# Optimization experiments

Measured on AMD Instinct MI355X. Metric: run time of the kernel, lower is better.

The kernel has to match this reference:

```python
import jax, jax.numpy as jnp
import numpy as np

KNN_K = 10        # init kwarg knn_k
EPS_COS = 1e-8    # torch F.cosine_similarity default eps
EPS_SCALE = 1e-6  # clamp on median displacement variance


def _knn_indices(pts, k):
    """pts: [B, P, 3]. Returns [B, P, k] indices of nearest points.

    Matches torch: topk over negative squared pairwise distance (self point
    has distance 0 and is therefore included among the neighbors).
    """
    inner = jnp.einsum('bpd,bqd->bpq', pts, pts)            # [B,P,P]
    xx = jnp.sum(pts * pts, axis=-1)                        # [B,P]
    neg_dist = 2.0 * inner - xx[:, :, None] - xx[:, None, :]
    return jax.lax.top_k(neg_dist, k)[1]                    # [B,P,k]


def setup_inputs() -> dict:
    key = jax.random.key(0)
    k1, k2 = jax.random.split(key)
    B, D, T, P = 4, 128, 8, 4096
    return {
        'encoded': jax.random.normal(k1, (B, D, T * P), dtype=jnp.float32),
        'points_4d': jax.random.normal(k2, (B, T, P, 4), dtype=jnp.float32),
        'num_frames': T,
        'pts_per_frame': P,
    }


def reference(encoded, points_4d, num_frames, pts_per_frame):
    B, D, _ = encoded.shape
    xyz = points_4d[..., :3]                                # [B,T,P,3]
    feat = encoded.reshape(B, D, num_frames, pts_per_frame)
    k = min(KNN_K, pts_per_frame - 1)
    gather = jax.vmap(lambda a, i: a[i])                    # per-batch fancy gather

    total = jnp.asarray(0.0, dtype=encoded.dtype)
    for t in range(num_frames - 1):                         # small fixed frame loop
        pts = xyz[:, t]                                     # [B,P,3]
        disp = xyz[:, t + 1] - pts                          # [B,P,3]
        idx = _knn_indices(pts, k)                          # [B,P,k]

        nbr_disp = gather(disp, idx)                        # [B,P,k,3]
        disp_diff = nbr_disp - disp[:, :, None, :]
        disp_var = jnp.mean(jnp.sum(disp_diff * disp_diff, axis=-1), axis=-1)  # [B,P]

        # torch .median() on even-length returns the lower middle element
        flat = jnp.sort(disp_var.reshape(-1))
        scale = jnp.maximum(flat[(flat.shape[0] - 1) // 2], EPS_SCALE)
        rigidity = jax.lax.stop_gradient(jnp.exp(-disp_var / scale))  # detached

        feat_t = jnp.transpose(feat[:, :, t], (0, 2, 1))    # [B,P,D]
        nbr_feat = gather(feat_t, idx)                      # [B,P,k,D]
        num = jnp.einsum('bpd,bpkd->bpk', feat_t, nbr_feat)
        nq = jnp.maximum(jnp.linalg.norm(feat_t, axis=-1), EPS_COS)   # [B,P]
        nn_ = jnp.maximum(jnp.linalg.norm(nbr_feat, axis=-1), EPS_COS)  # [B,P,k]
        cos_sim = num / (nq[:, :, None] * nn_)
        mean_sim = jnp.mean(cos_sim, axis=-1)               # [B,P]

        total = total + jnp.mean(rigidity * (1.0 - mean_sim))
    return total / max(num_frames - 1, 1)
```

## Files before the change

### kernel.cpp

```cpp
#include <hip/hip_runtime.h>
#include <math.h>

#define BB 4
#define DD 128
#define TT 8
#define PP 4096
#define KK 10
#define NT 7
#define BP (BB*PP)
#define NQ (NT*BP)
#define NBLK_COS 896
#define QPB 128

#define CHUNKS 4
#define CSZ (PP/CHUNKS)
#define SELCAP 16

#define OFF_FEATT 0u
#define OFF_PARTV 0u
#define OFF_CAND4 20971520u
#define OFF_IDX   58720256u
#define OFF_DV    63307776u
#define OFF_NORM  63766528u
#define OFF_SCALE 64225280u
#define OFF_PART  64225536u

typedef __fp16 f16x2 __attribute__((ext_vector_type(2)));
union H2U { f16x2 h; unsigned u; };

__device__ __forceinline__ float md_of(const float4 q, const float4 c) {
  float s = q.w + c.w;
  float inner = fmaf(q.x, c.x, fmaf(q.y, c.y, q.z * c.z));
  return fmaf(-2.0f, inner, s);
}

__device__ __forceinline__ void ins2(f16x2 (&bv)[KK], float mdA, float mdB) {
  H2U cv;
  cv.h = __builtin_amdgcn_cvt_pkrtz(mdA, mdB);
  cv.u += 0x00020002u;
  bv[KK - 1] = __builtin_elementwise_min(bv[KK - 1], cv.h);
#pragma unroll
  for (int i = KK - 1; i > 0; --i) {
    f16x2 lo = __builtin_elementwise_min(bv[i - 1], bv[i]);
    f16x2 hi = __builtin_elementwise_max(bv[i - 1], bv[i]);
    bv[i - 1] = lo;
    bv[i] = hi;
  }
}
__device__ __forceinline__ void insh(f16x2 (&bv)[KK], f16x2 h) {
  bv[KK - 1] = __builtin_elementwise_min(bv[KK - 1], h);
#pragma unroll
  for (int i = KK - 1; i > 0; --i) {
    f16x2 lo = __builtin_elementwise_min(bv[i - 1], bv[i]);
    f16x2 hi = __builtin_elementwise_max(bv[i - 1], bv[i]);
    bv[i - 1] = lo;
    bv[i] = hi;
  }
}

__device__ __forceinline__ void insf(float (&bv)[KK], float v) {
  bv[KK - 1] = fminf(bv[KK - 1], v);
#pragma unroll
  for (int i = KK - 1; i > 0; --i) {
    float lo = fminf(bv[i - 1], bv[i]);
    float hi = fmaxf(bv[i - 1], bv[i]);
    bv[i - 1] = lo;
    bv[i] = hi;
  }
}

__device__ __forceinline__ void insp(float (&v)[KK], int (&vi)[KK], float md,
                                     int j) {
  bool en = md < v[KK - 1];
  v[KK - 1] = en ? md : v[KK - 1];
  vi[KK - 1] = en ? j : vi[KK - 1];
#pragma unroll
  for (int i = KK - 1; i > 0; --i) {
    bool sw = v[i] < v[i - 1];
    float tv = sw ? v[i - 1] : v[i];
    v[i - 1] = sw ? v[i] : v[i - 1];
    v[i] = tv;
    int ti = sw ? vi[i - 1] : vi[i];
    vi[i - 1] = sw ? vi[i] : vi[i - 1];
    vi[i] = ti;
  }
}

__device__ __forceinline__ void rec16(int (&a)[SELCAP], int cnt, int j) {
#pragma unroll
  for (int r = 0; r < SELCAP; ++r) a[r] = (cnt == r) ? j : a[r];
}

__global__ __launch_bounds__(256) void prep_cand(
    const float* __restrict__ pts4, float4* __restrict__ cand4) {
  const int i = blockIdx.x * 256 + threadIdx.x;
  float4 v = ((const float4*)pts4)[i];
  v.w = fmaf(v.x, v.x, fmaf(v.y, v.y, v.z * v.z));
  cand4[i] = v;
}

__global__ __launch_bounds__(256) void knn_thr_partial(
    const float4* __restrict__ cand4, unsigned* __restrict__ part) {
  const int qg = blockIdx.x >> 2;
  const int c = blockIdx.x & 3;
  const int b = blockIdx.y, t = blockIdx.z;
  const float4* __restrict__ src = cand4 + ((size_t)(b * TT + t) * PP);
  const float4* __restrict__ ch = src + c * CSZ;

  const int p = qg * 256 + threadIdx.x;
  const float4 q = src[p];

  H2U inf2;
  inf2.u = 0x7C007C00u;
  f16x2 l1[KK], l2[KK];
#pragma unroll
  for (int i = 0; i < KK; ++i) { l1[i] = inf2.h; l2[i] = inf2.h; }

  for (int j = 0; j < CSZ; j += 4) {
    float4 c0 = ch[j], c1 = ch[j + 1], c2 = ch[j + 2], c3 = ch[j + 3];
    float md0 = md_of(q, c0);
    float md1 = md_of(q, c1);
    float md2 = md_of(q, c2);
    float md3 = md_of(q, c3);
    ins2(l1, md0, md1);
    ins2(l2, md2, md3);
  }
#pragma unroll
  for (int r = 0; r < KK; ++r) insh(l1, l2[r]);

  const size_t qid = (size_t)(t * BB + b) * PP + p;
#pragma unroll
  for (int r = 0; r < KK; ++r) {
    H2U w;
    w.h = l1[r];
    part[(size_t)(c * KK + r) * NQ + qid] = w.u;
  }
}

__global__ __launch_bounds__(256) void knn_collect(
    const float4* __restrict__ cand4, const float* __restrict__ pts4,
    const unsigned* __restrict__ part, int* __restrict__ idx_out,
    float* __restrict__ dv_out) {
  __shared__ float4 cand[PP];
  const int qg = blockIdx.x;
  const int b = blockIdx.y, t = blockIdx.z;
  const float4* __restrict__ src = cand4 + ((size_t)(b * TT + t) * PP);
  const float4* __restrict__ src1 =
      (const float4*)pts4 + ((size_t)(b * TT + t + 1) * PP);

  for (int i = threadIdx.x; i < PP; i += 256) cand[i] = src[i];
  __syncthreads();

  const int p = qg * 256 + threadIdx.x;
  const size_t g = (size_t)(t * BB + b) * PP + p;

  float bv[KK];
#pragma unroll
  for (int i = 0; i < KK; ++i) bv[i] = INFINITY;
#pragma unroll
  for (int c = 0; c < CHUNKS; ++c) {
#pragma unroll
    for (int r = 0; r < KK; ++r) {
      H2U w;
      w.u = part[(size_t)(c * KK + r) * NQ + g];
      insf(bv, (float)w.h.x);
      insf(bv, (float)w.h.y);
    }
  }
  const float tau = bv[KK - 1] + 1e-4f;

  const float4 q = cand[p];

  int sel[SELCAP];
#pragma unroll
  for (int r = 0; r < SELCAP; ++r) sel[r] = 0;
  int cnt = 0;

  for (int j = 0; j < PP; j += 8) {
    float4 c0 = cand[j], c1 = cand[j + 1], c2 = cand[j + 2], c3 = cand[j + 3];
    float4 c4 = cand[j + 4], c5 = cand[j + 5], c6 = cand[j + 6],
           c7 = cand[j + 7];
    float m0 = md_of(q, c0), m1 = md_of(q, c1), m2 = md_of(q, c2),
          m3 = md_of(q, c3);
    float m4 = md_of(q, c4), m5 = md_of(q, c5), m6 = md_of(q, c6),
          m7 = md_of(q, c7);
#define FLT(mm, jj)                          \
    if ((mm) <= tau) { rec16(sel, cnt, (jj)); ++cnt; }
    FLT(m0, j); FLT(m1, j + 1); FLT(m2, j + 2); FLT(m3, j + 3);
    FLT(m4, j + 4); FLT(m5, j + 5); FLT(m6, j + 6); FLT(m7, j + 7);
#undef FLT
  }

  float v[KK];
  int vi[KK];
#pragma unroll
  for (int i = 0; i < KK; ++i) { v[i] = INFINITY; vi[i] = 0; }
  const int m = cnt < SELCAP ? cnt : SELCAP;
#pragma unroll
  for (int r = 0; r < SELCAP; ++r) {
    if (r < m) {
      int j = sel[r];
      insp(v, vi, md_of(q, cand[j]), j);
    }
  }

  float4 a1 = src1[p];
  const float dqx = a1.x - q.x, dqy = a1.y - q.y, dqz = a1.z - q.z;
  float s = 0.0f;
  int* myidx = idx_out + g * KK;
#pragma unroll
  for (int r = 0; r < KK; ++r) {
    int j = vi[r];
    float4 cc = cand[j];
    float4 n1 = src1[j];
    float dx = (n1.x - cc.x) - dqx;
    float dy = (n1.y - cc.y) - dqy;
    float dz = (n1.z - cc.z) - dqz;
    s += fmaf(dx, dx, fmaf(dy, dy, dz * dz));
    myidx[r] = j;
  }
  dv_out[g] = s * (1.0f / KK);
}

__global__ __launch_bounds__(256) void transpose_kernel(
    const float* __restrict__ encoded, float* __restrict__ featT) {
  __shared__ float tile[32][33];
  const int slice = blockIdx.z;
  const int t = slice / BB, b = slice % BB;
  const int p0 = blockIdx.x * 32, d0 = blockIdx.y * 32;
  const int tx = threadIdx.x, ty = threadIdx.y;
#pragma unroll
  for (int r = 0; r < 4; ++r) {
    int d = d0 + ty + r * 8;
    tile[ty + r * 8][tx] =
        encoded[((size_t)(b * DD + d)) * (TT * PP) + (size_t)t * PP + p0 + tx];
  }
  __syncthreads();
#pragma unroll
  for (int r = 0; r < 4; ++r) {
    int p = p0 + ty + r * 8;
    featT[((size_t)slice * PP + p) * DD + d0 + tx] = tile[tx][ty + r * 8];
  }
}

__global__ __launch_bounds__(256) void norms_kernel(
    const float* __restrict__ featT, float* __restrict__ norms) {
  const int w = threadIdx.x >> 6, lane = threadIdx.x & 63;
  const int wid = blockIdx.x * 4 + w;
  for (int i = 0; i < 32; ++i) {
    const int g = wid * 32 + i;
    float2 f = *(const float2*)(featT + (size_t)g * DD + lane * 2);
    float part = fmaf(f.x, f.x, f.y * f.y);
#pragma unroll
    for (int o = 32; o > 0; o >>= 1) part += __shfl_xor(part, o);
    if (lane == 0) norms[g] = sqrtf(part);
  }
}

__global__ __launch_bounds__(256) void median_kernel(
    const float* __restrict__ disp_var, float* __restrict__ scale) {
  const int t = blockIdx.x;
  const unsigned* u = (const unsigned*)(disp_var + (size_t)t * BP);
  __shared__ unsigned hist[256];
  __shared__ unsigned sh_prefix;
  __shared__ int sh_rank;
  if (threadIdx.x == 0) { sh_prefix = 0u; sh_rank = (BP - 1) >> 1; }
  __syncthreads();
  for (int pass = 0; pass < 4; ++pass) {
    const int shift = 24 - pass * 8;
    hist[threadIdx.x] = 0u;
    __syncthreads();
    const unsigned hmask = (pass == 0) ? 0u : (0xFFFFFFFFu << (shift + 8));
    const unsigned prefix = sh_prefix;
    for (int i = threadIdx.x; i < BP; i += 256) {
      unsigned v = u[i];
      if ((v & hmask) == prefix) atomicAdd(&hist[(v >> shift) & 255u], 1u);
    }
    __syncthreads();
    if (threadIdx.x == 0) {
      int rank = sh_rank;
      unsigned run = 0u;
      for (int c = 0; c < 256; ++c) {
        unsigned h = hist[c];
        if (run + h > (unsigned)rank) {
          sh_rank = rank - (int)run;
          sh_prefix = prefix | ((unsigned)c << shift);
          break;
        }
        run += h;
      }
    }
    __syncthreads();
  }
  if (threadIdx.x == 0) {
    float med = __uint_as_float(sh_prefix);
    scale[t] = fmaxf(med, 1e-6f);
  }
}

__global__ __launch_bounds__(256) void cos_loss_kernel(
    const float* __restrict__ featT, const int* __restrict__ idxw,
    const float* __restrict__ norms, const float* __restrict__ dv,
    const float* __restrict__ scale, float* __restrict__ partial) {
  const int w = threadIdx.x >> 6, lane = threadIdx.x & 63;
  __shared__ float wsum[4];
  float acc = 0.0f;
  const int qbase = blockIdx.x * QPB + w * (QPB / 4);
  for (int i = 0; i < QPB / 4; ++i) {
    const int g = qbase + i;
    const int t = g >> 14;
    const int p = g & (PP - 1);
    const int slice = g - p;
    const float* fbase = featT + (size_t)g * DD;
    float2 fq = *(const float2*)(fbase + lane * 2);
    float nq = fmaxf(norms[g], 1e-8f);
    const int* ip = idxw + (size_t)g * KK;
    float msum = 0.0f;
#pragma unroll
    for (int k = 0; k < KK; ++k) {
      int j = ip[k];
      const float* nb = featT + (size_t)(slice + j) * DD;
      float2 fn = *(const float2*)(nb + lane * 2);
      float part = fmaf(fq.x, fn.x, fq.y * fn.y);
#pragma unroll
      for (int o = 32; o > 0; o >>= 1) part += __shfl_xor(part, o);
      float nn = fmaxf(norms[slice + j], 1e-8f);
      msum += part / (nq * nn);
    }
    float mean_sim = msum * (1.0f / KK);
    float rig = expf(-dv[g] / scale[t]);
    acc += rig * (1.0f - mean_sim);
  }
  if (lane == 0) wsum[w] = acc;
  __syncthreads();
  if (threadIdx.x == 0)
    partial[blockIdx.x] = (wsum[0] + wsum[1]) + (wsum[2] + wsum[3]);
}

__global__ __launch_bounds__(256) void final_reduce_kernel(
    const float* __restrict__ partial, float* __restrict__ out) {
  __shared__ float sh[256];
  float s = 0.0f;
  for (int i = threadIdx.x; i < NBLK_COS; i += 256) s += partial[i];
  sh[threadIdx.x] = s;
  __syncthreads();
  for (int st = 128; st > 0; st >>= 1) {
    if (threadIdx.x < st) sh[threadIdx.x] += sh[threadIdx.x + st];
    __syncthreads();
  }
  if (threadIdx.x == 0) out[0] = sh[0] * (1.0f / (float)NQ);
}

extern "C" void kernel_launch(void* const* d_in, const int* in_sizes, int n_in,
                              void* d_out, int out_size, void* d_ws,
                              size_t ws_size, hipStream_t stream) {
  const float* encoded = (const float*)d_in[0];
  const float* pts4 = (const float*)d_in[1];
  char* ws = (char*)d_ws;
  float* featT = (float*)(ws + OFF_FEATT);
  unsigned* part = (unsigned*)(ws + OFF_PARTV);
  float4* cand4 = (float4*)(ws + OFF_CAND4);
  int* idxw = (int*)(ws + OFF_IDX);
  float* dv = (float*)(ws + OFF_DV);
  float* norms = (float*)(ws + OFF_NORM);
  float* scale = (float*)(ws + OFF_SCALE);
  float* partial = (float*)(ws + OFF_PART);
  float* outp = (float*)d_out;

  prep_cand<<<(BB * TT * PP) / 256, 256, 0, stream>>>(pts4, cand4);
  knn_thr_partial<<<dim3(16 * CHUNKS, BB, NT), 256, 0, stream>>>(cand4, part);
  knn_collect<<<dim3(16, BB, NT), 256, 0, stream>>>(cand4, pts4, part, idxw,
                                                    dv);
  transpose_kernel<<<dim3(PP / 32, DD / 32, NT * BB), dim3(32, 8), 0, stream>>>(
      encoded, featT);
  norms_kernel<<<NBLK_COS, 256, 0, stream>>>(featT, norms);
  median_kernel<<<NT, 256, 0, stream>>>(dv, scale);
  cos_loss_kernel<<<NBLK_COS, 256, 0, stream>>>(featT, idxw, norms, dv, scale,
                                                partial);
  final_reduce_kernel<<<1, 256, 0, stream>>>(partial, outp);
}
```

Measured before the change: 785.0 us.

## Split KNN collect into tau, chunked filter, and finish kernels

Replaces the single knn_collect kernel, which ran only 448 blocks and scanned all 4096 candidates per query from shared memory, with three kernels. A tau kernel computes the per-query threshold, a filter kernel scans candidates in four chunks across four times as many blocks and records up to 12 survivors per chunk, and a finish kernel merges the survivors into the exact top-k. The aim is more parallelism and occupancy for the brute-force scan. In exchange it adds two launches and extra global traffic for the threshold, counts and candidate lists, and it loses the shared-memory candidate cache.

```diff
diff --git a/kernel.cpp b/kernel.cpp
--- a/kernel.cpp
+++ b/kernel.cpp
@@ -14,11 +14,14 @@
 
 #define CHUNKS 4
 #define CSZ (PP/CHUNKS)
-#define SELCAP 16
+#define FCAP 12
 
 #define OFF_FEATT 0u
 #define OFF_PARTV 0u
 #define OFF_CAND4 20971520u
+#define OFF_TAU   23068672u
+#define OFF_FCNT  23527424u
+#define OFF_FLIST 25362432u
 #define OFF_IDX   58720256u
 #define OFF_DV    63307776u
 #define OFF_NORM  63766528u
@@ -86,9 +89,9 @@
   }
 }
 
-__device__ __forceinline__ void rec16(int (&a)[SELCAP], int cnt, int j) {
-#pragma unroll
-  for (int r = 0; r < SELCAP; ++r) a[r] = (cnt == r) ? j : a[r];
+__device__ __forceinline__ void rec12(int (&a)[FCAP], int cnt, int j) {
+#pragma unroll
+  for (int r = 0; r < FCAP; ++r) a[r] = (cnt == r) ? j : a[r];
 }
 
 __global__ __launch_bounds__(256) void prep_cand(
@@ -137,23 +140,9 @@
   }
 }
 
-__global__ __launch_bounds__(256) void knn_collect(
-    const float4* __restrict__ cand4, const float* __restrict__ pts4,
-    const unsigned* __restrict__ part, int* __restrict__ idx_out,
-    float* __restrict__ dv_out) {
-  __shared__ float4 cand[PP];
-  const int qg = blockIdx.x;
-  const int b = blockIdx.y, t = blockIdx.z;
-  const float4* __restrict__ src = cand4 + ((size_t)(b * TT + t) * PP);
-  const float4* __restrict__ src1 =
-      (const float4*)pts4 + ((size_t)(b * TT + t + 1) * PP);
-
-  for (int i = threadIdx.x; i < PP; i += 256) cand[i] = src[i];
-  __syncthreads();
-
-  const int p = qg * 256 + threadIdx.x;
-  const size_t g = (size_t)(t * BB + b) * PP + p;
-
+__global__ __launch_bounds__(256) void tau_kernel(
+    const unsigned* __restrict__ part, float* __restrict__ tau_arr) {
+  const int g = blockIdx.x * 256 + threadIdx.x;
   float bv[KK];
 #pragma unroll
   for (int i = 0; i < KK; ++i) bv[i] = INFINITY;
@@ -167,51 +156,90 @@
       insf(bv, (float)w.h.y);
     }
   }
-  const float tau = bv[KK - 1] + 1e-4f;
-
-  const float4 q = cand[p];
-
-  int sel[SELCAP];
-#pragma unroll
-  for (int r = 0; r < SELCAP; ++r) sel[r] = 0;
+  tau_arr[g] = bv[KK - 1] + 1e-4f;
+}
+
+__global__ __launch_bounds__(256) void knn_filter(
+    const float4* __restrict__ cand4, const float* __restrict__ tau_arr,
+    unsigned* __restrict__ fcnt, unsigned short* __restrict__ flist) {
+  const int qg = blockIdx.x >> 2;
+  const int c = blockIdx.x & 3;
+  const int b = blockIdx.y, t = blockIdx.z;
+  const float4* __restrict__ src = cand4 + ((size_t)(b * TT + t) * PP);
+  const float4* __restrict__ ch = src + c * CSZ;
+  const int jbase = c * CSZ;
+
+  const int p = qg * 256 + threadIdx.x;
+  const size_t g = (size_t)(t * BB + b) * PP + p;
+  const float4 q = src[p];
+  const float tau = tau_arr[g];
+
+  int sel[FCAP];
+#pragma unroll
+  for (int r = 0; r < FCAP; ++r) sel[r] = 0;
   int cnt = 0;
 
-  for (int j = 0; j < PP; j += 8) {
-    float4 c0 = cand[j], c1 = cand[j + 1], c2 = cand[j + 2], c3 = cand[j + 3];
-    float4 c4 = cand[j + 4], c5 = cand[j + 5], c6 = cand[j + 6],
-           c7 = cand[j + 7];
+  for (int j = 0; j < CSZ; j += 8) {
+    float4 c0 = ch[j], c1 = ch[j + 1], c2 = ch[j + 2], c3 = ch[j + 3];
+    float4 c4 = ch[j + 4], c5 = ch[j + 5], c6 = ch[j + 6], c7 = ch[j + 7];
     float m0 = md_of(q, c0), m1 = md_of(q, c1), m2 = md_of(q, c2),
           m3 = md_of(q, c3);
     float m4 = md_of(q, c4), m5 = md_of(q, c5), m6 = md_of(q, c6),
           m7 = md_of(q, c7);
-#define FLT(mm, jj)                          \
-    if ((mm) <= tau) { rec16(sel, cnt, (jj)); ++cnt; }
+#define FLT(mm, jj)                                         \
+    if ((mm) <= tau) { rec12(sel, cnt, jbase + (jj)); ++cnt; }
     FLT(m0, j); FLT(m1, j + 1); FLT(m2, j + 2); FLT(m3, j + 3);
     FLT(m4, j + 4); FLT(m5, j + 5); FLT(m6, j + 6); FLT(m7, j + 7);
 #undef FLT
   }
 
+  fcnt[(size_t)c * NQ + g] = (unsigned)cnt;
+#pragma unroll
+  for (int r = 0; r < FCAP; ++r)
+    flist[(size_t)(c * FCAP + r) * NQ + g] = (unsigned short)sel[r];
+}
+
+__global__ __launch_bounds__(256) void knn_finish(
+    const float4* __restrict__ cand4, const float* __restrict__ pts4,
+    const unsigned* __restrict__ fcnt, const unsigned short* __restrict__ flist,
+    int* __restrict__ idx_out, float* __restrict__ dv_out) {
+  const int g = blockIdx.x * 256 + threadIdx.x;
+  const int t = g >> 14;
+  const int rem = g & (BP - 1);
+  const int b = rem >> 12;
+  const int p = rem & (PP - 1);
+  const float4* __restrict__ src = cand4 + ((size_t)(b * TT + t) * PP);
+  const float4* __restrict__ src1 =
+      (const float4*)pts4 + ((size_t)(b * TT + t + 1) * PP);
+
+  const float4 q = src[p];
+
   float v[KK];
   int vi[KK];
 #pragma unroll
   for (int i = 0; i < KK; ++i) { v[i] = INFINITY; vi[i] = 0; }
-  const int m = cnt < SELCAP ? cnt : SELCAP;
-#pragma unroll
-  for (int r = 0; r < SELCAP; ++r) {
-    if (r < m) {
-      int j = sel[r];
-      insp(v, vi, md_of(q, cand[j]), j);
+
+#pragma unroll
+  for (int c = 0; c < CHUNKS; ++c) {
+    int cn = (int)fcnt[(size_t)c * NQ + g];
+    cn = cn < FCAP ? cn : FCAP;
+#pragma unroll
+    for (int r = 0; r < FCAP; ++r) {
+      if (r < cn) {
+        int j = (int)flist[(size_t)(c * FCAP + r) * NQ + g];
+        insp(v, vi, md_of(q, src[j]), j);
+      }
     }
   }
 
   float4 a1 = src1[p];
   const float dqx = a1.x - q.x, dqy = a1.y - q.y, dqz = a1.z - q.z;
   float s = 0.0f;
-  int* myidx = idx_out + g * KK;
+  int* myidx = idx_out + (size_t)g * KK;
 #pragma unroll
   for (int r = 0; r < KK; ++r) {
     int j = vi[r];
-    float4 cc = cand[j];
+    float4 cc = src[j];
     float4 n1 = src1[j];
     float dx = (n1.x - cc.x) - dqx;
     float dy = (n1.y - cc.y) - dqy;
@@ -360,6 +388,9 @@
   float* featT = (float*)(ws + OFF_FEATT);
   unsigned* part = (unsigned*)(ws + OFF_PARTV);
   float4* cand4 = (float4*)(ws + OFF_CAND4);
+  float* tau_arr = (float*)(ws + OFF_TAU);
+  unsigned* fcnt = (unsigned*)(ws + OFF_FCNT);
+  unsigned short* flist = (unsigned short*)(ws + OFF_FLIST);
   int* idxw = (int*)(ws + OFF_IDX);
   float* dv = (float*)(ws + OFF_DV);
   float* norms = (float*)(ws + OFF_NORM);
@@ -369,8 +400,10 @@
 
   prep_cand<<<(BB * TT * PP) / 256, 256, 0, stream>>>(pts4, cand4);
   knn_thr_partial<<<dim3(16 * CHUNKS, BB, NT), 256, 0, stream>>>(cand4, part);
-  knn_collect<<<dim3(16, BB, NT), 256, 0, stream>>>(cand4, pts4, part, idxw,
-                                                    dv);
+  tau_kernel<<<NQ / 256, 256, 0, stream>>>(part, tau_arr);
+  knn_filter<<<dim3(16 * CHUNKS, BB, NT), 256, 0, stream>>>(cand4, tau_arr,
+                                                            fcnt, flist);
+  knn_finish<<<NQ / 256, 256, 0, stream>>>(cand4, pts4, fcnt, flist, idxw, dv);
   transpose_kernel<<<dim3(PP / 32, DD / 32, NT * BB), dim3(32, 8), 0, stream>>>(
       encoded, featT);
   norms_kernel<<<NBLK_COS, 256, 0, stream>>>(featT, norms);
```

Result: faster. 737.7 us (-6.0%).
